# Kernel optimization log

Measured on AMD Instinct MI355X. Metric: run time of the kernel, lower is better.

Reference implementation:

```python
import jax, jax.numpy as jnp
import numpy as np

THRESHOLD = 0.0  # default float threshold, non-learned path
SURROGATE_TAU = 0.1

@jax.custom_vjp
def jumprelu(x):
    # Forward: hard threshold x * 1[x > THRESHOLD]
    return x * (x > THRESHOLD).astype(x.dtype)

def _jumprelu_fwd(x):
    return jumprelu(x), x

def _jumprelu_bwd(x, g):
    # Smooth surrogate gradient of x * sigmoid(x/tau)
    tau = SURROGATE_TAU
    sig = jax.nn.sigmoid(x / tau)
    surrogate = sig + x * sig * (1.0 - sig) / tau
    return (g * surrogate,)

jumprelu.defvjp(_jumprelu_fwd, _jumprelu_bwd)

NUM_TRANSFORMS = 64
D_MODEL = 2048
RANK = 32
BATCH = 2048

def setup_inputs() -> dict:
    key = jax.random.key(0)
    kx, kv, ku, ke = jax.random.split(key, 4)
    scale = (1.0 / (D_MODEL * RANK)) ** 0.25
    x = jax.random.normal(kx, (BATCH, D_MODEL), dtype=jnp.float32)
    V = jax.random.normal(kv, (NUM_TRANSFORMS, RANK, D_MODEL), dtype=jnp.float32) * scale
    U = jax.random.normal(ku, (NUM_TRANSFORMS, D_MODEL, RANK), dtype=jnp.float32) * scale
    encoder = jax.random.normal(ke, (NUM_TRANSFORMS, D_MODEL), dtype=jnp.float32)
    encoder = encoder / jnp.linalg.norm(encoder, axis=1, keepdims=True)
    bias = jnp.full((NUM_TRANSFORMS,), -1.0, dtype=jnp.float32)
    return {"x": x, "V": V, "U": U, "encoder": encoder, "bias": bias}

def reference(x, V, U, encoder, bias):
    # pre_acts: (batch, num_transforms)
    pre_acts = x @ encoder.T - bias
    gate = jumprelu(pre_acts)
    # Vx: (n, b, r); UVx: (n, b, d)
    Vx = jnp.einsum('nrd,bd->nbr', V, x)
    UVx = jnp.einsum('ndr,nbr->nbd', U, Vx)
    gated = UVx * gate.T[:, :, None]
    output = gated.sum(axis=0)  # (batch, d_model)
    u_norms = jnp.linalg.norm(U.reshape(U.shape[0], -1), axis=1)
    v_norms = jnp.linalg.norm(V.reshape(V.shape[0], -1), axis=1)
    frobenius_norms = u_norms * v_norms / (D_MODEL * RANK) ** 0.5
    return (output, gate, frobenius_norms)
```

## Files before the change

### kernel.cpp

```cpp
#include <hip/hip_runtime.h>


#define D_MODEL 2048
#define BATCH   2048
#define NT      64
#define RANK    32

typedef __attribute__((ext_vector_type(8))) __bf16 bf16x8;
typedef __attribute__((ext_vector_type(4))) float  f32x4;

__device__ __forceinline__ unsigned short f2bf(float f) {
  unsigned int u = __builtin_bit_cast(unsigned int, f);
  u += 0x7FFFu + ((u >> 16) & 1u);
  return (unsigned short)(u >> 16);
}

__device__ __forceinline__ void gload_lds16(const void* g, void* l) {
  __builtin_amdgcn_global_load_lds(
      (const __attribute__((address_space(1))) unsigned int*)g,
      (__attribute__((address_space(3))) unsigned int*)l,
      16, 0, 0);
}


__global__ void k_convert(const float4* __restrict__ in, ushort4* __restrict__ out, int n4) {
  int i = blockIdx.x * blockDim.x + threadIdx.x;
  int stride = gridDim.x * blockDim.x;
  for (; i < n4; i += stride) {
    float4 v = in[i];
    ushort4 o;
    o.x = f2bf(v.x); o.y = f2bf(v.y); o.z = f2bf(v.z); o.w = f2bf(v.w);
    out[i] = o;
  }
}

__device__ __forceinline__ void block_reduce_store(float ss, float* dst) {
  __shared__ float red[256];
  int t = threadIdx.x;
  red[t] = ss;
  __syncthreads();
  for (int s = 128; s > 0; s >>= 1) {
    if (t < s) red[t] += red[t + s];
    __syncthreads();
  }
  if (t == 0) dst[blockIdx.x] = red[0];
}

__global__ void k_conv_v(const float4* __restrict__ V, ushort4* __restrict__ Vb,
                         float* __restrict__ partV) {
  int bid = blockIdx.x, t = threadIdx.x;
  size_t base4 = (size_t)bid * 4096;
  float ss = 0.f;
  for (int it = 0; it < 16; ++it) {
    size_t idx = base4 + t + it * 256;
    float4 v = V[idx];
    ss += v.x * v.x + v.y * v.y + v.z * v.z + v.w * v.w;
    ushort4 o;
    o.x = f2bf(v.x); o.y = f2bf(v.y); o.z = f2bf(v.z); o.w = f2bf(v.w);
    Vb[idx] = o;
  }
  block_reduce_store(ss, partV);
}

__global__ void k_conv_u(const float4* __restrict__ U, unsigned short* __restrict__ Ut,
                         float* __restrict__ partU) {
  int bid = blockIdx.x, t = threadIdx.x;
  int n = bid >> 2;
  size_t base4 = (size_t)bid * 4096;
  float ss = 0.f;
  for (int it = 0; it < 16; ++it) {
    size_t idx4 = base4 + t + it * 256;
    float4 v = U[idx4];
    ss += v.x * v.x + v.y * v.y + v.z * v.z + v.w * v.w;
    size_t e = idx4 * 4 - (size_t)n * (D_MODEL * RANK);
    int dcol = (int)(e >> 5);
    int r = (int)(e & 31);
    ushort4 o;
    o.x = f2bf(v.x); o.y = f2bf(v.y); o.z = f2bf(v.z); o.w = f2bf(v.w);
    *(ushort4*)(Ut + (size_t)dcol * 2048 + n * 32 + r) = o;
  }
  block_reduce_store(ss, partU);
}

__global__ void k_frob(const float* __restrict__ pU, const float* __restrict__ pV,
                       float* __restrict__ frob) {
  int n = threadIdx.x;
  if (n < NT) {
    float su = pU[4 * n] + pU[4 * n + 1] + pU[4 * n + 2] + pU[4 * n + 3];
    float sv = pV[4 * n] + pV[4 * n + 1] + pV[4 * n + 2] + pV[4 * n + 3];
    frob[n] = sqrtf(su) * sqrtf(sv) * (1.0f / 256.0f);
  }
}

__global__ void k_gate_reduce(const float* __restrict__ part, const float* __restrict__ bias,
                              float* __restrict__ gate) {
  int t = threadIdx.x;
#pragma unroll
  for (int u = 0; u < 4; ++u) {
    int idx = blockIdx.x * 1024 + u * 256 + t;
    float s = 0.f;
#pragma unroll
    for (int z = 0; z < 8; ++z) s += part[(size_t)z * (BATCH * NT) + idx];
    float pre = s - bias[idx & (NT - 1)];
    gate[idx] = pre > 0.f ? pre : 0.f;
  }
}

template <int WGM, int WGN, int MI, int NJ, int EPI>
__global__ void gemm_bt(const unsigned short* __restrict__ A,
                        const unsigned short* __restrict__ Bt,
                        const float* __restrict__ aux,
                        unsigned short* __restrict__ outB,
                        float* __restrict__ outF, int K, int klen) {
  constexpr int BM = WGM * MI * 16;
  constexpr int BN = WGN * NJ * 16;
  constexpr int RA = BM / 32;
  constexpr int RB = BN / 32;
  __shared__ __align__(16) unsigned short smem[(BM + BN) * 64];
  unsigned short* As = smem;
  unsigned short* Bs = smem + BM * 64;

  const int tid = threadIdx.x;
  const int w = tid >> 6;
  const int lane = tid & 63;
  const int quad = lane >> 4;
  const int l15 = lane & 15;
  const int wm = w % WGM;
  const int wn = w / WGM;
  const int blockN = blockIdx.x, blockM = blockIdx.y;
  const int kbeg = blockIdx.z * klen;

  const int lrow = lane >> 3;
  const int lq = (lane & 7) ^ lrow;
  const unsigned short* Ag = A + (size_t)(blockM * BM + lrow) * K + kbeg + lq * 8;
  const unsigned short* Bg = Bt + (size_t)(blockN * BN + lrow) * K + kbeg + lq * 8;

  const int pcs = (quad ^ (lane & 7)) * 16;
  const int rfA = wm * MI * 16 + l15;
  const int rfB = wn * NJ * 16 + l15;

  f32x4 acc[MI][NJ];
  const f32x4 z = {0.f, 0.f, 0.f, 0.f};
#pragma unroll
  for (int i = 0; i < MI; ++i)
#pragma unroll
    for (int j = 0; j < NJ; ++j) acc[i][j] = z;

  for (int k0 = 0; k0 < klen; k0 += 64) {
#pragma unroll
    for (int j = 0; j < RA; ++j)
      gload_lds16(Ag + (size_t)((j * 4 + w) * 8) * K + k0,
                  (char*)As + (j * 4 + w) * 1024);
#pragma unroll
    for (int j = 0; j < RB; ++j)
      gload_lds16(Bg + (size_t)((j * 4 + w) * 8) * K + k0,
                  (char*)Bs + (j * 4 + w) * 1024);
    __syncthreads();
#pragma unroll
    for (int s = 0; s < 2; ++s) {
      bf16x8 af[MI], bfr[NJ];
#pragma unroll
      for (int i = 0; i < MI; ++i)
        af[i] = *(const bf16x8*)((const char*)As + (rfA + i * 16) * 128 + (pcs ^ (s << 6)));
#pragma unroll
      for (int j = 0; j < NJ; ++j)
        bfr[j] = *(const bf16x8*)((const char*)Bs + (rfB + j * 16) * 128 + (pcs ^ (s << 6)));
#pragma unroll
      for (int i = 0; i < MI; ++i)
#pragma unroll
        for (int j = 0; j < NJ; ++j)
          acc[i][j] = __builtin_amdgcn_mfma_f32_16x16x32_bf16(af[i], bfr[j], acc[i][j], 0, 0, 0);
    }
    __syncthreads();
  }

  const int row0 = blockM * BM + wm * MI * 16 + quad * 4;
  const int col0 = blockN * BN + wn * NJ * 16 + l15;
#pragma unroll
  for (int i = 0; i < MI; ++i) {
#pragma unroll
    for (int j = 0; j < NJ; ++j) {
      const int col = col0 + j * 16;
#pragma unroll
      for (int t = 0; t < 4; ++t) {
        const int row = row0 + i * 16 + t;
        float v = acc[i][j][t];
        if constexpr (EPI == 0) {
          float g = aux[(size_t)row * NT + (col >> 5)];
          outB[(size_t)row * 2048 + col] = f2bf(v * g);
        } else if constexpr (EPI == 1) {
          outF[(size_t)row * 2048 + col] = v;
        } else {
          outF[(size_t)blockIdx.z * (BATCH * NT) + (size_t)row * NT + col] = v;
        }
      }
    }
  }
}


extern "C" void kernel_launch(void* const* d_in, const int* in_sizes, int n_in,
                              void* d_out, int out_size, void* d_ws, size_t ws_size,
                              hipStream_t stream) {
  const float* x    = (const float*)d_in[0];
  const float* V    = (const float*)d_in[1];
  const float* U    = (const float*)d_in[2];
  const float* enc  = (const float*)d_in[3];
  const float* bias = (const float*)d_in[4];

  float* out  = (float*)d_out;
  float* gate = out + (size_t)BATCH * D_MODEL;
  float* frob = gate + (size_t)BATCH * NT;

  char* ws = (char*)d_ws;
  unsigned short* xb   = (unsigned short*)(ws);
  unsigned short* Vb   = (unsigned short*)(ws + (8u << 20));
  unsigned short* Ut   = (unsigned short*)(ws + (16u << 20));
  unsigned short* Yg   = (unsigned short*)(ws + (24u << 20));
  float* gatePart      = (float*)Yg;
  unsigned short* encb = (unsigned short*)(ws + (32u << 20));
  float* partU = (float*)(ws + (32u << 20) + 262144);
  float* partV = partU + 256;

  k_convert<<<1024, 256, 0, stream>>>((const float4*)x, (ushort4*)xb, BATCH * D_MODEL / 4);
  k_convert<<<128, 256, 0, stream>>>((const float4*)enc, (ushort4*)encb, NT * D_MODEL / 4);
  k_conv_v<<<256, 256, 0, stream>>>((const float4*)V, (ushort4*)Vb, partV);
  k_conv_u<<<256, 256, 0, stream>>>((const float4*)U, Ut, partU);
  k_frob<<<1, 64, 0, stream>>>(partU, partV, frob);

  gemm_bt<4, 1, 2, 4, 3><<<dim3(1, 16, 8), 256, 0, stream>>>(
      xb, encb, nullptr, nullptr, gatePart, D_MODEL, 256);
  k_gate_reduce<<<128, 256, 0, stream>>>(gatePart, bias, gate);

  gemm_bt<2, 2, 4, 2, 0><<<dim3(32, 16, 1), 256, 0, stream>>>(
      xb, Vb, gate, Yg, nullptr, D_MODEL, D_MODEL);

  gemm_bt<2, 2, 4, 2, 1><<<dim3(32, 16, 1), 256, 0, stream>>>(
      Yg, Ut, nullptr, nullptr, out, D_MODEL, D_MODEL);
}
```

Before: 180.7 us.

## Fuse prep kernels into one launch and add XCD-aware block swizzle for GEMMs

Merges the x, encoder, V and U conversion kernels into a single k_prep launch dispatched by block range. The Frobenius-norm finalisation moves into the gate-reduce kernel. The two large GEMMs now use a 1D grid remapped so that each XCD handles an 8x8 tile of output blocks, improving L2 locality of shared A/B panels. This is intended to cut launch overhead and redundant DRAM traffic, at the cost of a more branchy prep kernel.

New measurement: 166.4 us. 7.9% less time.

```diff
diff --git a/kernel.cpp b/kernel.cpp
--- a/kernel.cpp
+++ b/kernel.cpp
@@ -23,18 +23,7 @@
 }
 
 
-__global__ void k_convert(const float4* __restrict__ in, ushort4* __restrict__ out, int n4) {
-  int i = blockIdx.x * blockDim.x + threadIdx.x;
-  int stride = gridDim.x * blockDim.x;
-  for (; i < n4; i += stride) {
-    float4 v = in[i];
-    ushort4 o;
-    o.x = f2bf(v.x); o.y = f2bf(v.y); o.z = f2bf(v.z); o.w = f2bf(v.w);
-    out[i] = o;
-  }
-}
-
-__device__ __forceinline__ void block_reduce_store(float ss, float* dst) {
+__device__ __forceinline__ void block_reduce_store(float ss, float* dst, int slot) {
   __shared__ float red[256];
   int t = threadIdx.x;
   red[t] = ss;
@@ -43,58 +32,73 @@
     if (t < s) red[t] += red[t + s];
     __syncthreads();
   }
-  if (t == 0) dst[blockIdx.x] = red[0];
-}
-
-__global__ void k_conv_v(const float4* __restrict__ V, ushort4* __restrict__ Vb,
-                         float* __restrict__ partV) {
+  if (t == 0) dst[slot] = red[0];
+}
+
+__global__ void k_prep(const float4* __restrict__ x, const float4* __restrict__ enc,
+                       const float4* __restrict__ V, const float4* __restrict__ U,
+                       ushort4* __restrict__ xb, ushort4* __restrict__ encb,
+                       ushort4* __restrict__ Vb, unsigned short* __restrict__ Ut,
+                       float* __restrict__ partV, float* __restrict__ partU) {
   int bid = blockIdx.x, t = threadIdx.x;
-  size_t base4 = (size_t)bid * 4096;
-  float ss = 0.f;
-  for (int it = 0; it < 16; ++it) {
-    size_t idx = base4 + t + it * 256;
-    float4 v = V[idx];
-    ss += v.x * v.x + v.y * v.y + v.z * v.z + v.w * v.w;
+  if (bid < 1024) {
+#pragma unroll
+    for (int it = 0; it < 4; ++it) {
+      int i = bid * 1024 + it * 256 + t;
+      float4 v = x[i];
+      ushort4 o;
+      o.x = f2bf(v.x); o.y = f2bf(v.y); o.z = f2bf(v.z); o.w = f2bf(v.w);
+      xb[i] = o;
+    }
+  } else if (bid < 1152) {
+    int i = (bid - 1024) * 256 + t;
+    float4 v = enc[i];
     ushort4 o;
     o.x = f2bf(v.x); o.y = f2bf(v.y); o.z = f2bf(v.z); o.w = f2bf(v.w);
-    Vb[idx] = o;
-  }
-  block_reduce_store(ss, partV);
-}
-
-__global__ void k_conv_u(const float4* __restrict__ U, unsigned short* __restrict__ Ut,
-                         float* __restrict__ partU) {
-  int bid = blockIdx.x, t = threadIdx.x;
-  int n = bid >> 2;
-  size_t base4 = (size_t)bid * 4096;
-  float ss = 0.f;
-  for (int it = 0; it < 16; ++it) {
-    size_t idx4 = base4 + t + it * 256;
-    float4 v = U[idx4];
-    ss += v.x * v.x + v.y * v.y + v.z * v.z + v.w * v.w;
-    size_t e = idx4 * 4 - (size_t)n * (D_MODEL * RANK);
-    int dcol = (int)(e >> 5);
-    int r = (int)(e & 31);
-    ushort4 o;
-    o.x = f2bf(v.x); o.y = f2bf(v.y); o.z = f2bf(v.z); o.w = f2bf(v.w);
-    *(ushort4*)(Ut + (size_t)dcol * 2048 + n * 32 + r) = o;
-  }
-  block_reduce_store(ss, partU);
-}
-
-__global__ void k_frob(const float* __restrict__ pU, const float* __restrict__ pV,
-                       float* __restrict__ frob) {
-  int n = threadIdx.x;
-  if (n < NT) {
-    float su = pU[4 * n] + pU[4 * n + 1] + pU[4 * n + 2] + pU[4 * n + 3];
-    float sv = pV[4 * n] + pV[4 * n + 1] + pV[4 * n + 2] + pV[4 * n + 3];
-    frob[n] = sqrtf(su) * sqrtf(sv) * (1.0f / 256.0f);
+    encb[i] = o;
+  } else if (bid < 1408) {
+    int b = bid - 1152;
+    size_t base4 = (size_t)b * 4096;
+    float ss = 0.f;
+    for (int it = 0; it < 16; ++it) {
+      size_t idx = base4 + t + it * 256;
+      float4 v = V[idx];
+      ss += v.x * v.x + v.y * v.y + v.z * v.z + v.w * v.w;
+      ushort4 o;
+      o.x = f2bf(v.x); o.y = f2bf(v.y); o.z = f2bf(v.z); o.w = f2bf(v.w);
+      Vb[idx] = o;
+    }
+    block_reduce_store(ss, partV, b);
+  } else {
+    int b = bid - 1408;
+    int n = b >> 2;
+    size_t base4 = (size_t)b * 4096;
+    float ss = 0.f;
+    for (int it = 0; it < 16; ++it) {
+      size_t idx4 = base4 + t + it * 256;
+      float4 v = U[idx4];
+      ss += v.x * v.x + v.y * v.y + v.z * v.z + v.w * v.w;
+      size_t e = idx4 * 4 - (size_t)n * (D_MODEL * RANK);
+      int dcol = (int)(e >> 5);
+      int r = (int)(e & 31);
+      ushort4 o;
+      o.x = f2bf(v.x); o.y = f2bf(v.y); o.z = f2bf(v.z); o.w = f2bf(v.w);
+      *(ushort4*)(Ut + (size_t)dcol * 2048 + n * 32 + r) = o;
+    }
+    block_reduce_store(ss, partU, b);
   }
 }
 
 __global__ void k_gate_reduce(const float* __restrict__ part, const float* __restrict__ bias,
-                              float* __restrict__ gate) {
+                              float* __restrict__ gate,
+                              const float* __restrict__ pU, const float* __restrict__ pV,
+                              float* __restrict__ frob) {
   int t = threadIdx.x;
+  if (blockIdx.x == 0 && t < NT) {
+    float su = pU[4 * t] + pU[4 * t + 1] + pU[4 * t + 2] + pU[4 * t + 3];
+    float sv = pV[4 * t] + pV[4 * t + 1] + pV[4 * t + 2] + pV[4 * t + 3];
+    frob[t] = sqrtf(su) * sqrtf(sv) * (1.0f / 256.0f);
+  }
 #pragma unroll
   for (int u = 0; u < 4; ++u) {
     int idx = blockIdx.x * 1024 + u * 256 + t;
@@ -106,7 +110,7 @@
   }
 }
 
-template <int WGM, int WGN, int MI, int NJ, int EPI>
+template <int WGM, int WGN, int MI, int NJ, int EPI, int SWZ>
 __global__ void gemm_bt(const unsigned short* __restrict__ A,
                         const unsigned short* __restrict__ Bt,
                         const float* __restrict__ aux,
@@ -127,8 +131,20 @@
   const int l15 = lane & 15;
   const int wm = w % WGM;
   const int wn = w / WGM;
-  const int blockN = blockIdx.x, blockM = blockIdx.y;
-  const int kbeg = blockIdx.z * klen;
+
+  int blockM, blockN, kbeg;
+  if constexpr (SWZ) {
+    const int lin = blockIdx.x;
+    const int xcd = lin & 7;
+    const int i = lin >> 3;
+    blockM = (xcd & 1) * 8 + (i & 7);
+    blockN = (xcd >> 1) * 8 + (i >> 3);
+    kbeg = 0;
+  } else {
+    blockN = blockIdx.x;
+    blockM = blockIdx.y;
+    kbeg = blockIdx.z * klen;
+  }
 
   const int lrow = lane >> 3;
   const int lq = (lane & 7) ^ lrow;
@@ -222,19 +238,18 @@
   float* partU = (float*)(ws + (32u << 20) + 262144);
   float* partV = partU + 256;
 
-  k_convert<<<1024, 256, 0, stream>>>((const float4*)x, (ushort4*)xb, BATCH * D_MODEL / 4);
-  k_convert<<<128, 256, 0, stream>>>((const float4*)enc, (ushort4*)encb, NT * D_MODEL / 4);
-  k_conv_v<<<256, 256, 0, stream>>>((const float4*)V, (ushort4*)Vb, partV);
-  k_conv_u<<<256, 256, 0, stream>>>((const float4*)U, Ut, partU);
-  k_frob<<<1, 64, 0, stream>>>(partU, partV, frob);
-
-  gemm_bt<4, 1, 2, 4, 3><<<dim3(1, 16, 8), 256, 0, stream>>>(
+  k_prep<<<1664, 256, 0, stream>>>((const float4*)x, (const float4*)enc,
+                                   (const float4*)V, (const float4*)U,
+                                   (ushort4*)xb, (ushort4*)encb, (ushort4*)Vb, Ut,
+                                   partV, partU);
+
+  gemm_bt<4, 1, 2, 4, 3, 0><<<dim3(1, 16, 8), 256, 0, stream>>>(
       xb, encb, nullptr, nullptr, gatePart, D_MODEL, 256);
-  k_gate_reduce<<<128, 256, 0, stream>>>(gatePart, bias, gate);
-
-  gemm_bt<2, 2, 4, 2, 0><<<dim3(32, 16, 1), 256, 0, stream>>>(
+  k_gate_reduce<<<128, 256, 0, stream>>>(gatePart, bias, gate, partU, partV, frob);
+
+  gemm_bt<2, 2, 4, 2, 0, 1><<<512, 256, 0, stream>>>(
       xb, Vb, gate, Yg, nullptr, D_MODEL, D_MODEL);
 
-  gemm_bt<2, 2, 4, 2, 1><<<dim3(32, 16, 1), 256, 0, stream>>>(
+  gemm_bt<2, 2, 4, 2, 1, 1><<<512, 256, 0, stream>>>(
       Yg, Ut, nullptr, nullptr, out, D_MODEL, D_MODEL);
 }
```
